# Kernel optimization log

Hardware: AMD Instinct MI355X
Metric: run time of the kernel (lower is better)

Reference implementation:

```python
import jax, jax.numpy as jnp
import numpy as np

N, E, H, D_IN, D_HID, D_OUT = 50000, 800000, 2, 128, 64, 16
NEG_SLOPE = 0.2


def leaky(x, slope=NEG_SLOPE):
    return jnp.where(x >= 0, x, slope * x)


def gatv2_layer(x, src, dst, W_src, W_dst, attn, bias):
    # x: [N, Fin]; W_src/W_dst: [Fin, H*D]; attn: [H, D]; bias: [H*D]
    fs = (x @ W_src).reshape(-1, H, D_HID)  # source projection [N,H,D]
    fd = (x @ W_dst).reshape(-1, H, D_HID)  # dest projection   [N,H,D]
    e = leaky(fs[src] + fd[dst])             # [E,H,D] GATv2: LeakyReLU before attn dot
    logits = jnp.einsum('ehd,hd->eh', e, attn)  # [E,H]
    # edge softmax over incoming edges of each dst node
    m = jax.ops.segment_max(logits, dst, num_segments=N)  # [N,H]
    a = jnp.exp(logits - m[dst])
    s = jax.ops.segment_sum(a, dst, num_segments=N)       # [N,H]
    alpha = a / s[dst]                                     # [E,H]
    msg = fs[src] * alpha[..., None]                       # [E,H,D]
    out = jax.ops.segment_sum(msg, dst, num_segments=N)   # [N,H,D]
    return out.reshape(N, H * D_HID) + bias


def setup_inputs() -> dict:
    key = jax.random.key(0)
    ks = jax.random.split(key, 12)
    sc = 0.05
    return {
        'x': jax.random.normal(ks[0], (N, D_IN), jnp.float32),
        'src': jax.random.randint(ks[1], (E,), 0, N),
        'dst': jax.random.randint(ks[2], (E,), 0, N),
        'Wsrc0': jax.random.normal(ks[3], (D_IN, H * D_HID), jnp.float32) * sc,
        'Wdst0': jax.random.normal(ks[4], (D_IN, H * D_HID), jnp.float32) * sc,
        'attn0': jax.random.normal(ks[5], (H, D_HID), jnp.float32) * sc,
        'bias0': jnp.zeros((H * D_HID,), jnp.float32),
        'Wsrc1': jax.random.normal(ks[6], (H * D_HID, H * D_HID), jnp.float32) * sc,
        'Wdst1': jax.random.normal(ks[7], (H * D_HID, H * D_HID), jnp.float32) * sc,
        'attn1': jax.random.normal(ks[8], (H, D_HID), jnp.float32) * sc,
        'bias1': jnp.zeros((H * D_HID,), jnp.float32),
        'R0W': jax.random.normal(ks[9], (D_IN, D_OUT), jnp.float32) * sc,
        'R0b': jnp.zeros((D_OUT,), jnp.float32),
        'R1W': jax.random.normal(ks[10], (H * D_HID, D_OUT), jnp.float32) * sc,
        'R1b': jnp.zeros((D_OUT,), jnp.float32),
        'R2W': jax.random.normal(ks[11], (H * D_HID, D_OUT), jnp.float32) * sc,
        'R2b': jnp.zeros((D_OUT,), jnp.float32),
    }


def reference(x, src, dst, Wsrc0, Wdst0, attn0, bias0, Wsrc1, Wdst1, attn1, bias1,
              R0W, R0b, R1W, R1b, R2W, R2b):
    # eval mode: all dropouts / edge-drop are identity; norm='none'
    h0 = x
    h1 = leaky(gatv2_layer(h0, src, dst, Wsrc0, Wdst0, attn0, bias0))
    h2 = leaky(gatv2_layer(h1, src, dst, Wsrc1, Wdst1, attn1, bias1))
    # jumping-knowledge readout: sum of per-layer linear readouts
    score = (h0 @ R0W + R0b) + (h1 @ R1W + R1b) + (h2 @ R2W + R2b)
    return score
```

## Files before the change

kernel.cpp:

```cpp
#include <hip/hip_runtime.h>

#define NN 50000
#define NNP 50048
#define NE 800000
#define DF 128
#define BCAP 64

typedef __attribute__((ext_vector_type(8))) short short8v;
typedef __attribute__((ext_vector_type(4))) float float4v;
typedef __attribute__((ext_vector_type(2))) _Float16 half2v;

__device__ __forceinline__ float leaky(float t) { return fmaxf(t, 0.2f * t); }

__device__ __forceinline__ unsigned short rne_bf16(float x) {
  unsigned u = __float_as_uint(x);
  u = (u + 0x7fffu + ((u >> 16) & 1u)) >> 16;
  return (unsigned short)u;
}

__global__ void cast_all_kernel(const float* __restrict__ X, unsigned short* __restrict__ Xb,
                                const float* __restrict__ Ws0, const float* __restrict__ Wd0,
                                const float* __restrict__ Ws1, const float* __restrict__ Wd1,
                                unsigned short* __restrict__ WT0, unsigned short* __restrict__ WT1,
                                const float* __restrict__ R0W, const float* __restrict__ R1W,
                                const float* __restrict__ R2W, unsigned short* __restrict__ RT) {
  const int b = blockIdx.x;
  const int tid = threadIdx.x;
  if (b < 6250) {
    const int i = b * 256 + tid;
    const float4 v = ((const float4*)X)[i];
    uint2 o;
    o.x = rne_bf16(v.x) | ((unsigned)rne_bf16(v.y) << 16);
    o.y = rne_bf16(v.z) | ((unsigned)rne_bf16(v.w) << 16);
    ((uint2*)Xb)[i] = o;
  } else if (b < 6506) {
    const int idx = (b - 6250) * 256 + tid;
    const int l = idx >> 15;
    const int r = (idx >> 7) & 255;
    const int k = idx & 127;
    const float* Ws = l ? Ws1 : Ws0;
    const float* Wd = l ? Wd1 : Wd0;
    const float v = (r < 128) ? Ws[k * DF + r] : Wd[k * DF + (r - 128)];
    (l ? WT1 : WT0)[r * DF + k] = rne_bf16(v);
  } else {
    const int idx = (b - 6506) * 256 + tid;
    const int c = idx / 384, k = idx - c * 384;
    const float* Rw = (k < 128) ? R0W : (k < 256) ? R1W : R2W;
    RT[c * 384 + k] = rne_bf16(Rw[(k & 127) * 16 + c]);
  }
}

__global__ void hist_fill_kernel(const int* __restrict__ src, const int* __restrict__ dst,
                                 int* __restrict__ deg, unsigned short* __restrict__ ssrcB) {
  const int b = blockIdx.x;
  const int range = b & 7;
  const int e = (b >> 3) * 256 + threadIdx.x;
  const int dn = dst[e];
  const int sv = src[e];
  if (dn / 6250 != range) return;
  const int k = atomicAdd(&deg[dn], 1);
  if (k < BCAP) ssrcB[dn * BCAP + k] = (unsigned short)sv;
}

__global__ __launch_bounds__(256) void proj_mfma_kernel(const unsigned short* __restrict__ Ab,
                                                        const unsigned short* __restrict__ WT,
                                                        _Float16* __restrict__ fsh,
                                                        _Float16* __restrict__ fdh) {
  __shared__ unsigned short At[64][136];
  const int blk = blockIdx.x;
  const int tid = threadIdx.x;
  const int w = tid >> 6, l = tid & 63;

#pragma unroll
  for (int i = 0; i < 4; ++i) {
    const int flat = i * 256 + tid;
    const int r = flat >> 4, c16 = flat & 15;
    const int row = blk * 64 + r;
    uint4 v = make_uint4(0, 0, 0, 0);
    if (row < NN) v = ((const uint4*)Ab)[row * 16 + c16];
    *(uint4*)&At[r][c16 * 8] = v;
  }

  const int kof = (l >> 4) * 8;
  const int cbase = w * 64 + (l & 15);
  short8v b[4][4];
#pragma unroll
  for (int ct = 0; ct < 4; ++ct)
#pragma unroll
    for (int kk = 0; kk < 4; ++kk)
      b[ct][kk] = *(const short8v*)(WT + (cbase + ct * 16) * DF + kk * 32 + kof);
  __syncthreads();

  const int lrow = l & 15;
#pragma unroll
  for (int rt = 0; rt < 4; ++rt) {
    short8v a[4];
#pragma unroll
    for (int kk = 0; kk < 4; ++kk) a[kk] = *(const short8v*)&At[rt * 16 + lrow][kk * 32 + kof];
    const int r0 = blk * 64 + rt * 16 + (l >> 4) * 4;
#pragma unroll
    for (int ct = 0; ct < 4; ++ct) {
      float4v acc = {0.f, 0.f, 0.f, 0.f};
#pragma unroll
      for (int kk = 0; kk < 4; ++kk)
        acc = __builtin_amdgcn_mfma_f32_16x16x32_bf16(a[kk], b[ct][kk], acc, 0, 0, 0);
      const int col = cbase + ct * 16;
      _Float16* O = (col < DF) ? fsh : fdh;
      const int c2 = (col < DF) ? col : col - DF;
#pragma unroll
      for (int r = 0; r < 4; ++r)
        if (r0 + r < NN) O[(r0 + r) * DF + c2] = (_Float16)acc[r];
    }
  }
}

__global__ __launch_bounds__(256) void csr_attention_kernel(
    const _Float16* __restrict__ fsh, const _Float16* __restrict__ fdh,
    const float* __restrict__ attn, const int* __restrict__ degv,
    const unsigned short* __restrict__ ssrcB, const float* __restrict__ bias,
    unsigned short* __restrict__ houtb) {
  const int node = (blockIdx.x * 256 + threadIdx.x) >> 6;
  const int lane = threadIdx.x & 63;
  const int eg = lane >> 4, s16 = lane & 15;
  const int deg = min(degv[node], BCAP);
  const unsigned short* __restrict__ sb = ssrcB + node * BCAP;

  half2v fdv[4], at[4];
  {
    const uint4 fq = ((const uint4*)fdh)[node * 16 + s16];
    fdv[0] = __builtin_bit_cast(half2v, fq.x);
    fdv[1] = __builtin_bit_cast(half2v, fq.y);
    fdv[2] = __builtin_bit_cast(half2v, fq.z);
    fdv[3] = __builtin_bit_cast(half2v, fq.w);
    const float4 a0 = ((const float4*)(attn + s16 * 8))[0];
    const float4 a1 = ((const float4*)(attn + s16 * 8))[1];
    const float l2e = 1.44269504f;
    at[0] = (half2v){(_Float16)(a0.x * l2e), (_Float16)(a0.y * l2e)};
    at[1] = (half2v){(_Float16)(a0.z * l2e), (_Float16)(a0.w * l2e)};
    at[2] = (half2v){(_Float16)(a1.x * l2e), (_Float16)(a1.y * l2e)};
    at[3] = (half2v){(_Float16)(a1.z * l2e), (_Float16)(a1.w * l2e)};
  }
  const half2v c02 = {(_Float16)0.2f, (_Float16)0.2f};

  float s = 0.f;
  half2v acc[4] = {{0, 0}, {0, 0}, {0, 0}, {0, 0}};
  const int nfull = deg >> 2;
  const int rem = deg & 3;

  int sn1 = (int)sb[min(eg, BCAP - 1)];
  uint4 q = ((const uint4*)fsh)[sn1 * 16 + s16];
  sn1 = (int)sb[min(eg + 4, BCAP - 1)];

  for (int j = 0; j < nfull; ++j) {
    const int sn2 = (int)sb[min(eg + 4 * j + 8, BCAP - 1)];
    const uint4 qn = ((const uint4*)fsh)[sn1 * 16 + s16];
    half2v f[4];
    f[0] = __builtin_bit_cast(half2v, q.x);
    f[1] = __builtin_bit_cast(half2v, q.y);
    f[2] = __builtin_bit_cast(half2v, q.z);
    f[3] = __builtin_bit_cast(half2v, q.w);
    float v = 0.f;
#pragma unroll
    for (int k = 0; k < 4; ++k) {
      const half2v t = f[k] + fdv[k];
      const half2v lk = __builtin_elementwise_max(t, t * c02);
      v = __builtin_amdgcn_fdot2(lk, at[k], v, false);
    }
    v += __shfl_xor(v, 1);
    v += __shfl_xor(v, 2);
    v += __shfl_xor(v, 4);
    const float p = exp2f(v);
    s += p;
    const _Float16 ph = (_Float16)p;
    const half2v p2 = {ph, ph};
#pragma unroll
    for (int k = 0; k < 4; ++k) acc[k] = p2 * f[k] + acc[k];
    sn1 = sn2;
    q = qn;
  }

  if (rem) {
    half2v f[4];
    f[0] = __builtin_bit_cast(half2v, q.x);
    f[1] = __builtin_bit_cast(half2v, q.y);
    f[2] = __builtin_bit_cast(half2v, q.z);
    f[3] = __builtin_bit_cast(half2v, q.w);
    float v = 0.f;
#pragma unroll
    for (int k = 0; k < 4; ++k) {
      const half2v t = f[k] + fdv[k];
      const half2v lk = __builtin_elementwise_max(t, t * c02);
      v = __builtin_amdgcn_fdot2(lk, at[k], v, false);
    }
    v += __shfl_xor(v, 1);
    v += __shfl_xor(v, 2);
    v += __shfl_xor(v, 4);
    const float p = (eg < rem) ? exp2f(v) : 0.f;
    s += p;
    const _Float16 ph = (_Float16)p;
    const half2v p2 = {ph, ph};
#pragma unroll
    for (int k = 0; k < 4; ++k) acc[k] = p2 * f[k] + acc[k];
  }

#pragma unroll
  for (int dist = 16; dist <= 32; dist <<= 1) {
    s += __shfl_xor(s, dist);
#pragma unroll
    for (int k = 0; k < 4; ++k) {
      const float of = __shfl_xor(__builtin_bit_cast(float, acc[k]), dist);
      acc[k] = acc[k] + __builtin_bit_cast(half2v, of);
    }
  }

  if (lane < 16) {
    const float rs = (deg > 0) ? 1.0f / s : 0.0f;
    const float4 b0 = ((const float4*)(bias + s16 * 8))[0];
    const float4 b1 = ((const float4*)(bias + s16 * 8))[1];
    const float bb[8] = {b0.x, b0.y, b0.z, b0.w, b1.x, b1.y, b1.z, b1.w};
    float ob[8];
#pragma unroll
    for (int k = 0; k < 4; ++k) {
      ob[2 * k]     = leaky(fmaf((float)acc[k].x, rs, bb[2 * k]));
      ob[2 * k + 1] = leaky(fmaf((float)acc[k].y, rs, bb[2 * k + 1]));
    }
    uint4 w;
    w.x = rne_bf16(ob[0]) | ((unsigned)rne_bf16(ob[1]) << 16);
    w.y = rne_bf16(ob[2]) | ((unsigned)rne_bf16(ob[3]) << 16);
    w.z = rne_bf16(ob[4]) | ((unsigned)rne_bf16(ob[5]) << 16);
    w.w = rne_bf16(ob[6]) | ((unsigned)rne_bf16(ob[7]) << 16);
    ((uint4*)houtb)[node * 16 + s16] = w;
  }
}

__global__ __launch_bounds__(256) void readout_mfma_kernel(
    const unsigned short* __restrict__ h0b, const unsigned short* __restrict__ h1b,
    const unsigned short* __restrict__ h2b, const unsigned short* __restrict__ RT,
    const float* __restrict__ R0b, const float* __restrict__ R1b,
    const float* __restrict__ R2b, float* __restrict__ out) {
  const int w = threadIdx.x >> 6, l = threadIdx.x & 63;
  const int row0 = blockIdx.x * 64 + w * 16;
  const int m = l & 15, ksub = (l >> 4) * 8;
  float4v acc = {0.f, 0.f, 0.f, 0.f};
  const unsigned short* hs[3] = {h0b, h1b, h2b};
#pragma unroll
  for (int a = 0; a < 3; ++a) {
    const unsigned short* __restrict__ H = hs[a];
#pragma unroll
    for (int kk = 0; kk < 4; ++kk) {
      const short8v av = *(const short8v*)(H + (size_t)(row0 + m) * DF + kk * 32 + ksub);
      const short8v bv = *(const short8v*)(RT + m * 384 + a * 128 + kk * 32 + ksub);
      acc = __builtin_amdgcn_mfma_f32_16x16x32_bf16(av, bv, acc, 0, 0, 0);
    }
  }
  const float rb = R0b[m] + R1b[m] + R2b[m];
  const int r0 = row0 + (l >> 4) * 4;
#pragma unroll
  for (int r = 0; r < 4; ++r)
    if (r0 + r < NN) out[(r0 + r) * 16 + m] = acc[r] + rb;
}

extern "C" void kernel_launch(void* const* d_in, const int* in_sizes, int n_in,
                              void* d_out, int out_size, void* d_ws, size_t ws_size,
                              hipStream_t stream) {
  const float* x     = (const float*)d_in[0];
  const int*   src   = (const int*)d_in[1];
  const int*   dst   = (const int*)d_in[2];
  const float* Wsrc0 = (const float*)d_in[3];
  const float* Wdst0 = (const float*)d_in[4];
  const float* attn0 = (const float*)d_in[5];
  const float* bias0 = (const float*)d_in[6];
  const float* Wsrc1 = (const float*)d_in[7];
  const float* Wdst1 = (const float*)d_in[8];
  const float* attn1 = (const float*)d_in[9];
  const float* bias1 = (const float*)d_in[10];
  const float* R0W   = (const float*)d_in[11];
  const float* R0b   = (const float*)d_in[12];
  const float* R1W   = (const float*)d_in[13];
  const float* R1b   = (const float*)d_in[14];
  const float* R2W   = (const float*)d_in[15];
  const float* R2b   = (const float*)d_in[16];
  float* out = (float*)d_out;

  unsigned short* xb  = (unsigned short*)d_ws;
  unsigned short* h1b = xb + (size_t)NNP * DF;
  unsigned short* h2b = h1b + (size_t)NNP * DF;
  _Float16* fsh = (_Float16*)(h2b + (size_t)NNP * DF);
  _Float16* fdh = fsh + (size_t)NN * DF;
  unsigned short* WT0 = (unsigned short*)(fdh + (size_t)NN * DF);
  unsigned short* WT1 = WT0 + 256 * DF;
  unsigned short* RT  = WT1 + 256 * DF;
  int* deg = (int*)(RT + 16 * 384);
  unsigned short* ssrcB = (unsigned short*)(deg + NN);

  hipMemsetAsync(deg, 0, NN * sizeof(int), stream);
  hist_fill_kernel<<<(NE / 256) * 8, 256, 0, stream>>>(src, dst, deg, ssrcB);

  cast_all_kernel<<<6530, 256, 0, stream>>>(x, xb, Wsrc0, Wdst0, Wsrc1, Wdst1, WT0, WT1,
                                            R0W, R1W, R2W, RT);

  const int prow = (NN + 63) / 64;
  proj_mfma_kernel<<<prow, 256, 0, stream>>>(xb, WT0, fsh, fdh);
  csr_attention_kernel<<<(NN * 64) / 256, 256, 0, stream>>>(fsh, fdh, attn0, deg, ssrcB, bias0, h1b);
  proj_mfma_kernel<<<prow, 256, 0, stream>>>(h1b, WT1, fsh, fdh);
  csr_attention_kernel<<<(NN * 64) / 256, 256, 0, stream>>>(fsh, fdh, attn1, deg, ssrcB, bias1, h2b);

  readout_mfma_kernel<<<NNP / 64, 256, 0, stream>>>(xb, h1b, h2b, RT, R0b, R1b, R2b, out);
}
```

Measured before the change: 173.5 us.

## Fuse input bf16 cast into projection and double-buffer attention gathers

The fp32-to-bf16 cast of x moves from the standalone cast kernel into the first projection kernel, which converts while loading its tile and also writes the bf16 copy for the readout. This removes one full read/write pass over x. The attention gather loop now keeps two outstanding feature loads per lane group instead of one, to hide more gather latency. The degree memset is replaced with a small zeroing kernel. The extra in-flight loads use more registers, which could lower occupancy.

```diff
diff --git a/kernel.cpp b/kernel.cpp
--- a/kernel.cpp
+++ b/kernel.cpp
@@ -18,23 +18,20 @@
   return (unsigned short)u;
 }
 
-__global__ void cast_all_kernel(const float* __restrict__ X, unsigned short* __restrict__ Xb,
-                                const float* __restrict__ Ws0, const float* __restrict__ Wd0,
-                                const float* __restrict__ Ws1, const float* __restrict__ Wd1,
-                                unsigned short* __restrict__ WT0, unsigned short* __restrict__ WT1,
-                                const float* __restrict__ R0W, const float* __restrict__ R1W,
-                                const float* __restrict__ R2W, unsigned short* __restrict__ RT) {
+__global__ void zero_deg_kernel(int* __restrict__ deg) {
+  const int i = blockIdx.x * 256 + threadIdx.x;
+  if (i < NN) deg[i] = 0;
+}
+
+__global__ void cast_w_kernel(const float* __restrict__ Ws0, const float* __restrict__ Wd0,
+                              const float* __restrict__ Ws1, const float* __restrict__ Wd1,
+                              unsigned short* __restrict__ WT0, unsigned short* __restrict__ WT1,
+                              const float* __restrict__ R0W, const float* __restrict__ R1W,
+                              const float* __restrict__ R2W, unsigned short* __restrict__ RT) {
   const int b = blockIdx.x;
   const int tid = threadIdx.x;
-  if (b < 6250) {
-    const int i = b * 256 + tid;
-    const float4 v = ((const float4*)X)[i];
-    uint2 o;
-    o.x = rne_bf16(v.x) | ((unsigned)rne_bf16(v.y) << 16);
-    o.y = rne_bf16(v.z) | ((unsigned)rne_bf16(v.w) << 16);
-    ((uint2*)Xb)[i] = o;
-  } else if (b < 6506) {
-    const int idx = (b - 6250) * 256 + tid;
+  if (b < 256) {
+    const int idx = b * 256 + tid;
     const int l = idx >> 15;
     const int r = (idx >> 7) & 255;
     const int k = idx & 127;
@@ -43,7 +40,7 @@
     const float v = (r < 128) ? Ws[k * DF + r] : Wd[k * DF + (r - 128)];
     (l ? WT1 : WT0)[r * DF + k] = rne_bf16(v);
   } else {
-    const int idx = (b - 6506) * 256 + tid;
+    const int idx = (b - 256) * 256 + tid;
     const int c = idx / 384, k = idx - c * 384;
     const float* Rw = (k < 128) ? R0W : (k < 256) ? R1W : R2W;
     RT[c * 384 + k] = rne_bf16(Rw[(k & 127) * 16 + c]);
@@ -63,6 +60,8 @@
 }
 
 __global__ __launch_bounds__(256) void proj_mfma_kernel(const unsigned short* __restrict__ Ab,
+                                                        const float* __restrict__ Xf,
+                                                        unsigned short* __restrict__ XbOut,
                                                         const unsigned short* __restrict__ WT,
                                                         _Float16* __restrict__ fsh,
                                                         _Float16* __restrict__ fdh) {
@@ -77,7 +76,19 @@
     const int r = flat >> 4, c16 = flat & 15;
     const int row = blk * 64 + r;
     uint4 v = make_uint4(0, 0, 0, 0);
-    if (row < NN) v = ((const uint4*)Ab)[row * 16 + c16];
+    if (Xf) {
+      if (row < NN) {
+        const float4 a = ((const float4*)Xf)[row * 32 + c16 * 2];
+        const float4 bq = ((const float4*)Xf)[row * 32 + c16 * 2 + 1];
+        v.x = rne_bf16(a.x) | ((unsigned)rne_bf16(a.y) << 16);
+        v.y = rne_bf16(a.z) | ((unsigned)rne_bf16(a.w) << 16);
+        v.z = rne_bf16(bq.x) | ((unsigned)rne_bf16(bq.y) << 16);
+        v.w = rne_bf16(bq.z) | ((unsigned)rne_bf16(bq.w) << 16);
+        ((uint4*)XbOut)[row * 16 + c16] = v;
+      }
+    } else {
+      if (row < NN) v = ((const uint4*)Ab)[row * 16 + c16];
+    }
     *(uint4*)&At[r][c16 * 8] = v;
   }
 
@@ -124,6 +135,7 @@
   const int eg = lane >> 4, s16 = lane & 15;
   const int deg = min(degv[node], BCAP);
   const unsigned short* __restrict__ sb = ssrcB + node * BCAP;
+  const uint4* __restrict__ fsh4 = (const uint4*)fsh;
 
   half2v fdv[4], at[4];
   {
@@ -147,13 +159,7 @@
   const int nfull = deg >> 2;
   const int rem = deg & 3;
 
-  int sn1 = (int)sb[min(eg, BCAP - 1)];
-  uint4 q = ((const uint4*)fsh)[sn1 * 16 + s16];
-  sn1 = (int)sb[min(eg + 4, BCAP - 1)];
-
-  for (int j = 0; j < nfull; ++j) {
-    const int sn2 = (int)sb[min(eg + 4 * j + 8, BCAP - 1)];
-    const uint4 qn = ((const uint4*)fsh)[sn1 * 16 + s16];
+  auto consume = [&](const uint4 q) {
     half2v f[4];
     f[0] = __builtin_bit_cast(half2v, q.x);
     f[1] = __builtin_bit_cast(half2v, q.y);
@@ -175,16 +181,36 @@
     const half2v p2 = {ph, ph};
 #pragma unroll
     for (int k = 0; k < 4; ++k) acc[k] = p2 * f[k] + acc[k];
-    sn1 = sn2;
-    q = qn;
-  }
-
+  };
+
+  int snA = (int)sb[min(eg, BCAP - 1)];
+  int snB = (int)sb[min(eg + 4, BCAP - 1)];
+  uint4 qA = fsh4[snA * 16 + s16];
+  uint4 qB = fsh4[snB * 16 + s16];
+  snA = (int)sb[min(eg + 8, BCAP - 1)];
+  snB = (int)sb[min(eg + 12, BCAP - 1)];
+
+  int base = eg + 16;
+  const int npairs = nfull >> 1;
+  for (int jj = 0; jj < npairs; ++jj) {
+    consume(qA);
+    qA = fsh4[snA * 16 + s16];
+    snA = (int)sb[min(base, BCAP - 1)];
+    consume(qB);
+    qB = fsh4[snB * 16 + s16];
+    snB = (int)sb[min(base + 4, BCAP - 1)];
+    base += 8;
+  }
+  if (nfull & 1) {
+    consume(qA);
+    qA = qB;
+  }
   if (rem) {
     half2v f[4];
-    f[0] = __builtin_bit_cast(half2v, q.x);
-    f[1] = __builtin_bit_cast(half2v, q.y);
-    f[2] = __builtin_bit_cast(half2v, q.z);
-    f[3] = __builtin_bit_cast(half2v, q.w);
+    f[0] = __builtin_bit_cast(half2v, qA.x);
+    f[1] = __builtin_bit_cast(half2v, qA.y);
+    f[2] = __builtin_bit_cast(half2v, qA.z);
+    f[3] = __builtin_bit_cast(half2v, qA.w);
     float v = 0.f;
 #pragma unroll
     for (int k = 0; k < 4; ++k) {
@@ -293,16 +319,16 @@
   int* deg = (int*)(RT + 16 * 384);
   unsigned short* ssrcB = (unsigned short*)(deg + NN);
 
-  hipMemsetAsync(deg, 0, NN * sizeof(int), stream);
+  zero_deg_kernel<<<(NN + 255) / 256, 256, 0, stream>>>(deg);
   hist_fill_kernel<<<(NE / 256) * 8, 256, 0, stream>>>(src, dst, deg, ssrcB);
 
-  cast_all_kernel<<<6530, 256, 0, stream>>>(x, xb, Wsrc0, Wdst0, Wsrc1, Wdst1, WT0, WT1,
-                                            R0W, R1W, R2W, RT);
+  cast_w_kernel<<<280, 256, 0, stream>>>(Wsrc0, Wdst0, Wsrc1, Wdst1, WT0, WT1,
+                                         R0W, R1W, R2W, RT);
 
   const int prow = (NN + 63) / 64;
-  proj_mfma_kernel<<<prow, 256, 0, stream>>>(xb, WT0, fsh, fdh);
+  proj_mfma_kernel<<<prow, 256, 0, stream>>>(nullptr, x, xb, WT0, fsh, fdh);
   csr_attention_kernel<<<(NN * 64) / 256, 256, 0, stream>>>(fsh, fdh, attn0, deg, ssrcB, bias0, h1b);
-  proj_mfma_kernel<<<prow, 256, 0, stream>>>(h1b, WT1, fsh, fdh);
+  proj_mfma_kernel<<<prow, 256, 0, stream>>>(h1b, nullptr, nullptr, WT1, fsh, fdh);
   csr_attention_kernel<<<(NN * 64) / 256, 256, 0, stream>>>(fsh, fdh, attn1, deg, ssrcB, bias1, h2b);
 
   readout_mfma_kernel<<<NNP / 64, 256, 0, stream>>>(xb, h1b, h2b, RT, R0b, R1b, R2b, out);
```

After: 162.0 us. -6.6%, faster.
